# Kernel tuning notes

Measured on AMD Instinct MI355X. Metric: run time of the kernel, lower is better.

## Reference

```python
import jax, jax.numpy as jnp
import numpy as np

N = 100000      # num_nodes
E = 1600000     # num_edges (avg degree 16)
IN = 128        # in_channels
HID = 8         # hidden_channels (per head)
HEADS = 8
OUT = 64        # out_channels
NEG_SLOPE = 0.2


def setup_inputs() -> dict:
    key = jax.random.key(0)
    ks = jax.random.split(key, 11)
    s = 0.05
    return {
        "x": jax.random.normal(ks[0], (N, IN), jnp.float32),
        "edge_index": jax.random.randint(ks[1], (2, E), 0, N, dtype=jnp.int32),
        "W1": jax.random.normal(ks[2], (IN, HEADS * HID), jnp.float32) * s,
        "a_src1": jax.random.normal(ks[3], (HEADS, HID), jnp.float32) * s,
        "a_dst1": jax.random.normal(ks[4], (HEADS, HID), jnp.float32) * s,
        "b1": jnp.zeros((HEADS * HID,), jnp.float32),
        "W2": jax.random.normal(ks[5], (HEADS * HID, OUT), jnp.float32) * s,
        "a_src2": jax.random.normal(ks[6], (1, OUT), jnp.float32) * s,
        "a_dst2": jax.random.normal(ks[7], (1, OUT), jnp.float32) * s,
        "b2": jnp.zeros((OUT,), jnp.float32),
    }


def gat_conv(x, src, dst, W, a_src, a_dst, bias, heads, out_ch):
    """PyG GATConv (concat=True, dropout=0, self-loops already in src/dst)."""
    n = x.shape[0]
    h = (x @ W).reshape(n, heads, out_ch)               # [N, H, C]
    al_src = jnp.einsum('nhc,hc->nh', h, a_src)          # [N, H]
    al_dst = jnp.einsum('nhc,hc->nh', h, a_dst)          # [N, H]
    e = jax.nn.leaky_relu(al_src[src] + al_dst[dst], NEG_SLOPE)  # [E, H]
    # segment softmax over destination nodes (numerically stable)
    e_max = jax.ops.segment_max(e, dst, num_segments=n)  # [N, H]
    ex = jnp.exp(e - e_max[dst])
    denom = jax.ops.segment_sum(ex, dst, num_segments=n)
    alpha = ex / (denom[dst] + 1e-16)                    # [E, H]
    msg = h[src] * alpha[:, :, None]                     # [E, H, C]
    out = jax.ops.segment_sum(msg, dst, num_segments=n)  # [N, H, C]
    return out.reshape(n, heads * out_ch) + bias


def reference(x, edge_index, W1, a_src1, a_dst1, b1, W2, a_src2, a_dst2, b2):
    n = x.shape[0]
    loops = jnp.arange(n, dtype=edge_index.dtype)
    src = jnp.concatenate([edge_index[0], loops])        # add self-loops (PyG default)
    dst = jnp.concatenate([edge_index[1], loops])
    h = gat_conv(x, src, dst, W1, a_src1, a_dst1, b1, HEADS, HID)
    h = jax.nn.elu(h)
    out = gat_conv(h, src, dst, W2, a_src2, a_dst2, b2, 1, OUT)
    return out
```

## Files before the change

### kernel.cpp

```cpp
#include <hip/hip_runtime.h>
#include <hip/hip_bf16.h>

#define IN_CH   128
#define HEADS   8
#define HID     8
#define MID_CH  64
#define OUT_CH  64
#define CAP     64
#define NRANGE  8

typedef unsigned short u16;
__device__ __forceinline__ u16 f2bu(float f) {
    union { float f; unsigned int i; } v; v.f = f;
    unsigned int lsb = (v.i >> 16) & 1u;
    return (u16)((v.i + 0x7fffu + lsb) >> 16);
}
__device__ __forceinline__ float2 up2(unsigned int u) {
    union { unsigned int i; float f; } a, b;
    a.i = u << 16; b.i = u & 0xffff0000u;
    return make_float2(a.f, b.f);
}
__device__ __forceinline__ float lrelu(float e) { return (e > 0.f) ? e : 0.2f * e; }

__global__ __launch_bounds__(256) void k1_fill(
    const int* __restrict__ src, const int* __restrict__ dst,
    int* __restrict__ deg, int* __restrict__ adj, int E, int N) {
    int range = blockIdx.x & (NRANGE - 1);
    int chunk = blockIdx.x >> 3;
    int lo = (int)(((long long)N * range) >> 3);
    int hi = (int)(((long long)N * (range + 1)) >> 3);
    int t = chunk * 256 + threadIdx.x;
    int base = t * 4;
    if (base + 3 < E) {
        int4 d4 = *(const int4*)(dst + base);
        bool ix = (d4.x >= lo && d4.x < hi);
        bool iy = (d4.y >= lo && d4.y < hi);
        bool iz = (d4.z >= lo && d4.z < hi);
        bool iw = (d4.w >= lo && d4.w < hi);
        if (ix | iy | iz | iw) {
            int4 s4 = *(const int4*)(src + base);
            if (ix) { int p = atomicAdd(&deg[d4.x], 1); if (p < CAP) adj[d4.x * CAP + p] = s4.x; }
            if (iy) { int p = atomicAdd(&deg[d4.y], 1); if (p < CAP) adj[d4.y * CAP + p] = s4.y; }
            if (iz) { int p = atomicAdd(&deg[d4.z], 1); if (p < CAP) adj[d4.z * CAP + p] = s4.z; }
            if (iw) { int p = atomicAdd(&deg[d4.w], 1); if (p < CAP) adj[d4.w * CAP + p] = s4.w; }
        }
    } else {
        for (int j = 0; j < 4; j++) {
            int e = base + j;
            if (e < E) {
                int d = dst[e];
                if (d >= lo && d < hi) {
                    int p = atomicAdd(&deg[d], 1);
                    if (p < CAP) adj[d * CAP + p] = src[e];
                }
            }
        }
    }
}

__global__ __launch_bounds__(256) void k2_gemm1(
    const float* __restrict__ x, const float* __restrict__ W1,
    const float* __restrict__ a_src, const float* __restrict__ a_dst,
    u16* __restrict__ h1b, float* __restrict__ als, float* __restrict__ ald, int N)
{
    __shared__ float Wl[IN_CH * MID_CH];
    __shared__ float xl[16 * IN_CH];
    int tid = threadIdx.x;
    {
        const float4* W4 = (const float4*)W1;
        float4* Wl4 = (float4*)Wl;
        #pragma unroll
        for (int i = tid; i < IN_CH * MID_CH / 4; i += 256) Wl4[i] = W4[i];
    }
    int base = blockIdx.x * 16;
    {
        float4* xl4 = (float4*)xl;
        const float4* x4 = (const float4*)x;
        #pragma unroll
        for (int i = tid; i < 16 * IN_CH / 4; i += 256) {
            int r = i >> 5;
            int n = base + r;
            xl4[i] = (n < N) ? x4[(size_t)n * (IN_CH / 4) + (i & 31)]
                             : make_float4(0.f, 0.f, 0.f, 0.f);
        }
    }
    __syncthreads();

    int wave = tid >> 6, lane = tid & 63;
    int r0 = wave * 4;
    const float* xr0 = &xl[(r0 + 0) * IN_CH];
    const float* xr1 = &xl[(r0 + 1) * IN_CH];
    const float* xr2 = &xl[(r0 + 2) * IN_CH];
    const float* xr3 = &xl[(r0 + 3) * IN_CH];
    float acc0 = 0.f, acc1 = 0.f, acc2 = 0.f, acc3 = 0.f;
    #pragma unroll 8
    for (int kc = 0; kc < IN_CH; kc += 4) {
        float4 xa = *(const float4*)(xr0 + kc);
        float4 xb = *(const float4*)(xr1 + kc);
        float4 xc = *(const float4*)(xr2 + kc);
        float4 xd = *(const float4*)(xr3 + kc);
        float w0 = Wl[(kc + 0) * MID_CH + lane];
        float w1 = Wl[(kc + 1) * MID_CH + lane];
        float w2 = Wl[(kc + 2) * MID_CH + lane];
        float w3 = Wl[(kc + 3) * MID_CH + lane];
        acc0 = fmaf(xa.x, w0, acc0); acc0 = fmaf(xa.y, w1, acc0);
        acc0 = fmaf(xa.z, w2, acc0); acc0 = fmaf(xa.w, w3, acc0);
        acc1 = fmaf(xb.x, w0, acc1); acc1 = fmaf(xb.y, w1, acc1);
        acc1 = fmaf(xb.z, w2, acc1); acc1 = fmaf(xb.w, w3, acc1);
        acc2 = fmaf(xc.x, w0, acc2); acc2 = fmaf(xc.y, w1, acc2);
        acc2 = fmaf(xc.z, w2, acc2); acc2 = fmaf(xc.w, w3, acc2);
        acc3 = fmaf(xd.x, w0, acc3); acc3 = fmaf(xd.y, w1, acc3);
        acc3 = fmaf(xd.z, w2, acc3); acc3 = fmaf(xd.w, w3, acc3);
    }
    float accs[4] = {acc0, acc1, acc2, acc3};
    float asv = a_src[lane];
    float adv = a_dst[lane];
    #pragma unroll
    for (int g = 0; g < 4; g++) {
        int n = base + r0 + g;
        if (n >= N) continue;
        h1b[(size_t)n * MID_CH + lane] = f2bu(accs[g]);
        float vs = accs[g] * asv;
        float vd = accs[g] * adv;
        vs += __shfl_xor(vs, 1); vs += __shfl_xor(vs, 2); vs += __shfl_xor(vs, 4);
        vd += __shfl_xor(vd, 1); vd += __shfl_xor(vd, 2); vd += __shfl_xor(vd, 4);
        if ((lane & 7) == 0) {
            als[n * HEADS + (lane >> 3)] = vs;
            ald[n * HEADS + (lane >> 3)] = vd;
        }
    }
}

__global__ __launch_bounds__(256) void k3_agg1(
    const int* __restrict__ deg, const int* __restrict__ adj,
    const u16* __restrict__ h1b, const float* __restrict__ als,
    const float* __restrict__ ald, const float* __restrict__ b1,
    float* __restrict__ h2, int N)
{
    __shared__ int adjl[4][CAP];
    int wave = threadIdx.x >> 6, lane = threadIdx.x & 63;
    int n = blockIdx.x * 4 + wave;
    bool valid = (n < N);
    int nc = valid ? n : (N - 1);

    int g = lane >> 3;
    int c8 = lane & 7;
    int dg = deg[nc]; if (dg > CAP) dg = CAP;
    if (lane < dg) adjl[wave][lane] = adj[(size_t)nc * CAP + lane];
    float aldv = ald[nc * HEADS + c8];
    __syncthreads();

    const uint4* h1v = (const uint4*)h1b;
    float acc[8] = {0,0,0,0,0,0,0,0};
    float denom = 0.f;
    for (int i = g; i < dg; i += 8) {
        int s = adjl[wave][i];
        float ex = __expf(lrelu(als[s * HEADS + c8] + aldv));
        uint4 q = h1v[(size_t)s * 8 + c8];
        float2 p0 = up2(q.x), p1 = up2(q.y), p2 = up2(q.z), p3 = up2(q.w);
        denom += ex;
        acc[0] += ex * p0.x; acc[1] += ex * p0.y;
        acc[2] += ex * p1.x; acc[3] += ex * p1.y;
        acc[4] += ex * p2.x; acc[5] += ex * p2.y;
        acc[6] += ex * p3.x; acc[7] += ex * p3.y;
    }
    if (g == 0) {
        float ex = __expf(lrelu(als[nc * HEADS + c8] + aldv));
        uint4 q = h1v[(size_t)nc * 8 + c8];
        float2 p0 = up2(q.x), p1 = up2(q.y), p2 = up2(q.z), p3 = up2(q.w);
        denom += ex;
        acc[0] += ex * p0.x; acc[1] += ex * p0.y;
        acc[2] += ex * p1.x; acc[3] += ex * p1.y;
        acc[4] += ex * p2.x; acc[5] += ex * p2.y;
        acc[6] += ex * p3.x; acc[7] += ex * p3.y;
    }
    denom += __shfl_xor(denom, 8); denom += __shfl_xor(denom, 16); denom += __shfl_xor(denom, 32);
    #pragma unroll
    for (int j = 0; j < 8; j++) {
        acc[j] += __shfl_xor(acc[j], 8);
        acc[j] += __shfl_xor(acc[j], 16);
        acc[j] += __shfl_xor(acc[j], 32);
    }
    float inv = 1.f / (denom + 1e-16f);

    if (g == 0 && valid) {
        const float4* b4 = (const float4*)b1;
        float4 bl = b4[c8 * 2], bh = b4[c8 * 2 + 1];
        float4 o0, o1;
        o0.x = acc[0] * inv + bl.x; o0.y = acc[1] * inv + bl.y;
        o0.z = acc[2] * inv + bl.z; o0.w = acc[3] * inv + bl.w;
        o1.x = acc[4] * inv + bh.x; o1.y = acc[5] * inv + bh.y;
        o1.z = acc[6] * inv + bh.z; o1.w = acc[7] * inv + bh.w;
        o0.x = (o0.x > 0.f) ? o0.x : (__expf(o0.x) - 1.f);
        o0.y = (o0.y > 0.f) ? o0.y : (__expf(o0.y) - 1.f);
        o0.z = (o0.z > 0.f) ? o0.z : (__expf(o0.z) - 1.f);
        o0.w = (o0.w > 0.f) ? o0.w : (__expf(o0.w) - 1.f);
        o1.x = (o1.x > 0.f) ? o1.x : (__expf(o1.x) - 1.f);
        o1.y = (o1.y > 0.f) ? o1.y : (__expf(o1.y) - 1.f);
        o1.z = (o1.z > 0.f) ? o1.z : (__expf(o1.z) - 1.f);
        o1.w = (o1.w > 0.f) ? o1.w : (__expf(o1.w) - 1.f);
        float4* h2v = (float4*)h2;
        h2v[(size_t)n * 16 + c8 * 2]     = o0;
        h2v[(size_t)n * 16 + c8 * 2 + 1] = o1;
    }
}

__global__ __launch_bounds__(256) void k4_gemm2(
    const float* __restrict__ h2, const float* __restrict__ W2,
    const float* __restrict__ a_src, const float* __restrict__ a_dst,
    u16* __restrict__ t2b, float* __restrict__ als, float* __restrict__ ald, int N)
{
    __shared__ float Wl[MID_CH * OUT_CH];
    __shared__ float xl[16 * MID_CH];
    int tid = threadIdx.x;
    {
        const float4* W4 = (const float4*)W2;
        float4* Wl4 = (float4*)Wl;
        #pragma unroll
        for (int i = tid; i < MID_CH * OUT_CH / 4; i += 256) Wl4[i] = W4[i];
    }
    int base = blockIdx.x * 16;
    {
        float4* xl4 = (float4*)xl;
        const float4* x4 = (const float4*)h2;
        #pragma unroll
        for (int i = tid; i < 16 * MID_CH / 4; i += 256) {
            int r = i >> 4;
            int n = base + r;
            xl4[i] = (n < N) ? x4[(size_t)n * (MID_CH / 4) + (i & 15)]
                             : make_float4(0.f, 0.f, 0.f, 0.f);
        }
    }
    __syncthreads();

    int wave = tid >> 6, lane = tid & 63;
    int r0 = wave * 4;
    const float* xr0 = &xl[(r0 + 0) * MID_CH];
    const float* xr1 = &xl[(r0 + 1) * MID_CH];
    const float* xr2 = &xl[(r0 + 2) * MID_CH];
    const float* xr3 = &xl[(r0 + 3) * MID_CH];
    float acc0 = 0.f, acc1 = 0.f, acc2 = 0.f, acc3 = 0.f;
    #pragma unroll 8
    for (int kc = 0; kc < MID_CH; kc += 4) {
        float4 xa = *(const float4*)(xr0 + kc);
        float4 xb = *(const float4*)(xr1 + kc);
        float4 xc = *(const float4*)(xr2 + kc);
        float4 xd = *(const float4*)(xr3 + kc);
        float w0 = Wl[(kc + 0) * OUT_CH + lane];
        float w1 = Wl[(kc + 1) * OUT_CH + lane];
        float w2 = Wl[(kc + 2) * OUT_CH + lane];
        float w3 = Wl[(kc + 3) * OUT_CH + lane];
        acc0 = fmaf(xa.x, w0, acc0); acc0 = fmaf(xa.y, w1, acc0);
        acc0 = fmaf(xa.z, w2, acc0); acc0 = fmaf(xa.w, w3, acc0);
        acc1 = fmaf(xb.x, w0, acc1); acc1 = fmaf(xb.y, w1, acc1);
        acc1 = fmaf(xb.z, w2, acc1); acc1 = fmaf(xb.w, w3, acc1);
        acc2 = fmaf(xc.x, w0, acc2); acc2 = fmaf(xc.y, w1, acc2);
        acc2 = fmaf(xc.z, w2, acc2); acc2 = fmaf(xc.w, w3, acc2);
        acc3 = fmaf(xd.x, w0, acc3); acc3 = fmaf(xd.y, w1, acc3);
        acc3 = fmaf(xd.z, w2, acc3); acc3 = fmaf(xd.w, w3, acc3);
    }
    float accs[4] = {acc0, acc1, acc2, acc3};
    float asv = a_src[lane];
    float adv = a_dst[lane];
    #pragma unroll
    for (int g = 0; g < 4; g++) {
        int n = base + r0 + g;
        if (n >= N) continue;
        t2b[(size_t)n * OUT_CH + lane] = f2bu(accs[g]);
        float vs = accs[g] * asv;
        float vd = accs[g] * adv;
        #pragma unroll
        for (int off = 1; off < 64; off <<= 1) {
            vs += __shfl_xor(vs, off);
            vd += __shfl_xor(vd, off);
        }
        if (lane == 0) { als[n] = vs; ald[n] = vd; }
    }
}

__global__ __launch_bounds__(256) void k5_agg2(
    const int* __restrict__ deg, const int* __restrict__ adj,
    const u16* __restrict__ t2b, const float* __restrict__ als,
    const float* __restrict__ ald, const float* __restrict__ b2,
    float* __restrict__ out, int N)
{
    __shared__ int adjl[4][CAP];
    int wave = threadIdx.x >> 6, lane = threadIdx.x & 63;
    int n = blockIdx.x * 4 + wave;
    bool valid = (n < N);
    int nc = valid ? n : (N - 1);

    int g = lane >> 3;
    int c8 = lane & 7;
    int dg = deg[nc]; if (dg > CAP) dg = CAP;
    if (lane < dg) adjl[wave][lane] = adj[(size_t)nc * CAP + lane];
    float aldv = ald[nc];
    __syncthreads();

    const uint4* t2v = (const uint4*)t2b;
    float acc[8] = {0,0,0,0,0,0,0,0};
    float denom = 0.f;
    for (int i = g; i < dg; i += 8) {
        int s = adjl[wave][i];
        float ex = __expf(lrelu(als[s] + aldv));
        uint4 q = t2v[(size_t)s * 8 + c8];
        float2 p0 = up2(q.x), p1 = up2(q.y), p2 = up2(q.z), p3 = up2(q.w);
        denom += ex;
        acc[0] += ex * p0.x; acc[1] += ex * p0.y;
        acc[2] += ex * p1.x; acc[3] += ex * p1.y;
        acc[4] += ex * p2.x; acc[5] += ex * p2.y;
        acc[6] += ex * p3.x; acc[7] += ex * p3.y;
    }
    if (g == 0) {
        float ex = __expf(lrelu(als[nc] + aldv));
        uint4 q = t2v[(size_t)nc * 8 + c8];
        float2 p0 = up2(q.x), p1 = up2(q.y), p2 = up2(q.z), p3 = up2(q.w);
        denom += ex;
        acc[0] += ex * p0.x; acc[1] += ex * p0.y;
        acc[2] += ex * p1.x; acc[3] += ex * p1.y;
        acc[4] += ex * p2.x; acc[5] += ex * p2.y;
        acc[6] += ex * p3.x; acc[7] += ex * p3.y;
    }
    denom += __shfl_xor(denom, 8); denom += __shfl_xor(denom, 16); denom += __shfl_xor(denom, 32);
    #pragma unroll
    for (int j = 0; j < 8; j++) {
        acc[j] += __shfl_xor(acc[j], 8);
        acc[j] += __shfl_xor(acc[j], 16);
        acc[j] += __shfl_xor(acc[j], 32);
    }
    float inv = 1.f / (denom + 1e-16f);

    if (g == 0 && valid) {
        const float4* b4 = (const float4*)b2;
        float4 bl = b4[c8 * 2], bh = b4[c8 * 2 + 1];
        float4 o0, o1;
        o0.x = acc[0] * inv + bl.x; o0.y = acc[1] * inv + bl.y;
        o0.z = acc[2] * inv + bl.z; o0.w = acc[3] * inv + bl.w;
        o1.x = acc[4] * inv + bh.x; o1.y = acc[5] * inv + bh.y;
        o1.z = acc[6] * inv + bh.z; o1.w = acc[7] * inv + bh.w;
        float4* ov = (float4*)out;
        ov[(size_t)n * 16 + c8 * 2]     = o0;
        ov[(size_t)n * 16 + c8 * 2 + 1] = o1;
    }
}

extern "C" void kernel_launch(void* const* d_in, const int* in_sizes, int n_in,
                              void* d_out, int out_size, void* d_ws, size_t ws_size,
                              hipStream_t stream) {
    const float* x   = (const float*)d_in[0];
    const int*   ei  = (const int*)d_in[1];
    const float* W1  = (const float*)d_in[2];
    const float* as1 = (const float*)d_in[3];
    const float* ad1 = (const float*)d_in[4];
    const float* b1  = (const float*)d_in[5];
    const float* W2  = (const float*)d_in[6];
    const float* as2 = (const float*)d_in[7];
    const float* ad2 = (const float*)d_in[8];
    const float* b2  = (const float*)d_in[9];
    float* out = (float*)d_out;

    int N = in_sizes[0] / IN_CH;
    int E = in_sizes[1] / 2;
    const int* srcp = ei;
    const int* dstp = ei + E;

    char* w = (char*)d_ws;
    size_t off = 0;
    auto alloc = [&](size_t bytes) {
        void* p = w + off;
        off += (bytes + 255) & ~(size_t)255;
        return p;
    };
    int*   deg  = (int*)  alloc((size_t)N * 4);
    int*   adj  = (int*)  alloc((size_t)N * CAP * 4);
    u16*   h1b  = (u16*)  alloc((size_t)N * MID_CH * 2);
    float* als1 = (float*)alloc((size_t)N * HEADS * 4);
    float* ald1 = (float*)alloc((size_t)N * HEADS * 4);
    float* h2   = (float*)alloc((size_t)N * MID_CH * 4);
    u16*   t2b  = (u16*)  alloc((size_t)N * OUT_CH * 2);
    float* als2 = (float*)alloc((size_t)N * 4);
    float* ald2 = (float*)alloc((size_t)N * 4);
    (void)ws_size; (void)n_in; (void)out_size;

    hipMemsetAsync(deg, 0, (size_t)N * 4, stream);
    int chunks = (E + 1023) / 1024;
    k1_fill<<<chunks * NRANGE, 256, 0, stream>>>(srcp, dstp, deg, adj, E, N);
    k2_gemm1<<<(N + 15) / 16, 256, 0, stream>>>(x, W1, as1, ad1, h1b, als1, ald1, N);
    k3_agg1<<<(N + 3) / 4, 256, 0, stream>>>(deg, adj, h1b, als1, ald1, b1, h2, N);
    k4_gemm2<<<(N + 15) / 16, 256, 0, stream>>>(h2, W2, as2, ad2, t2b, als2, ald2, N);
    k5_agg2<<<(N + 3) / 4, 256, 0, stream>>>(deg, adj, t2b, als2, ald2, b2, out, N);
}
```

Baseline: 370.3 us.

## Fuse adjacency fill into first GEMM kernel to overlap atomics with loads

Merges the edge-bucketing fill kernel into the layer-1 GEMM kernel. Each block handles two fill units: it issues the dst/src loads and the degree atomics before staging W1 and x into shared memory, then writes the adjacency entries afterwards, so atomic latency overlaps with the GEMM loads and one launch is removed. The grid is enlarged when needed to cover all fill units, and launch bounds now request 4 blocks per SM. This adds register pressure and relies on the GEMM path guarding blocks whose rows fall past N.

```diff
diff --git a/kernel.cpp b/kernel.cpp
--- a/kernel.cpp
+++ b/kernel.cpp
@@ -22,57 +22,77 @@
 }
 __device__ __forceinline__ float lrelu(float e) { return (e > 0.f) ? e : 0.2f * e; }
 
-__global__ __launch_bounds__(256) void k1_fill(
+#define FILL_ISSUE(U, D4, S4, P4)                                              \
+    do {                                                                        \
+        int range_ = (U) & (NRANGE - 1);                                        \
+        int chunk_ = (U) >> 3;                                                  \
+        int lo_ = (int)(((long long)N * range_) >> 3);                          \
+        int hi_ = (int)(((long long)N * (range_ + 1)) >> 3);                    \
+        int base_ = (chunk_ * 256 + threadIdx.x) * 4;                           \
+        if (base_ + 3 < E) {                                                    \
+            D4 = *(const int4*)(dst + base_);                                   \
+            bool ix_ = (D4.x >= lo_ && D4.x < hi_);                             \
+            bool iy_ = (D4.y >= lo_ && D4.y < hi_);                             \
+            bool iz_ = (D4.z >= lo_ && D4.z < hi_);                             \
+            bool iw_ = (D4.w >= lo_ && D4.w < hi_);                             \
+            if (ix_ | iy_ | iz_ | iw_) {                                        \
+                S4 = *(const int4*)(src + base_);                               \
+                if (ix_) P4.x = atomicAdd(&deg[D4.x], 1);                       \
+                if (iy_) P4.y = atomicAdd(&deg[D4.y], 1);                       \
+                if (iz_) P4.z = atomicAdd(&deg[D4.z], 1);                       \
+                if (iw_) P4.w = atomicAdd(&deg[D4.w], 1);                       \
+            }                                                                   \
+        } else {                                                                \
+            for (int j_ = 0; j_ < 4; j_++) {                                    \
+                int e_ = base_ + j_;                                            \
+                if (e_ < E) {                                                   \
+                    int d_ = dst[e_];                                           \
+                    if (d_ >= lo_ && d_ < hi_) {                                \
+                        int p_ = atomicAdd(&deg[d_], 1);                        \
+                        if (p_ < CAP) adj[(size_t)d_ * CAP + p_] = src[e_];     \
+                    }                                                           \
+                }                                                               \
+            }                                                                   \
+        }                                                                       \
+    } while (0)
+
+#define FILL_STORE(D4, S4, P4)                                                  \
+    do {                                                                        \
+        if (P4.x < CAP) adj[(size_t)D4.x * CAP + P4.x] = S4.x;                  \
+        if (P4.y < CAP) adj[(size_t)D4.y * CAP + P4.y] = S4.y;                  \
+        if (P4.z < CAP) adj[(size_t)D4.z * CAP + P4.z] = S4.z;                  \
+        if (P4.w < CAP) adj[(size_t)D4.w * CAP + P4.w] = S4.w;                  \
+    } while (0)
+
+__global__ __launch_bounds__(256, 4) void k12_fillgemm(
     const int* __restrict__ src, const int* __restrict__ dst,
-    int* __restrict__ deg, int* __restrict__ adj, int E, int N) {
-    int range = blockIdx.x & (NRANGE - 1);
-    int chunk = blockIdx.x >> 3;
-    int lo = (int)(((long long)N * range) >> 3);
-    int hi = (int)(((long long)N * (range + 1)) >> 3);
-    int t = chunk * 256 + threadIdx.x;
-    int base = t * 4;
-    if (base + 3 < E) {
-        int4 d4 = *(const int4*)(dst + base);
-        bool ix = (d4.x >= lo && d4.x < hi);
-        bool iy = (d4.y >= lo && d4.y < hi);
-        bool iz = (d4.z >= lo && d4.z < hi);
-        bool iw = (d4.w >= lo && d4.w < hi);
-        if (ix | iy | iz | iw) {
-            int4 s4 = *(const int4*)(src + base);
-            if (ix) { int p = atomicAdd(&deg[d4.x], 1); if (p < CAP) adj[d4.x * CAP + p] = s4.x; }
-            if (iy) { int p = atomicAdd(&deg[d4.y], 1); if (p < CAP) adj[d4.y * CAP + p] = s4.y; }
-            if (iz) { int p = atomicAdd(&deg[d4.z], 1); if (p < CAP) adj[d4.z * CAP + p] = s4.z; }
-            if (iw) { int p = atomicAdd(&deg[d4.w], 1); if (p < CAP) adj[d4.w * CAP + p] = s4.w; }
-        }
-    } else {
-        for (int j = 0; j < 4; j++) {
-            int e = base + j;
-            if (e < E) {
-                int d = dst[e];
-                if (d >= lo && d < hi) {
-                    int p = atomicAdd(&deg[d], 1);
-                    if (p < CAP) adj[d * CAP + p] = src[e];
-                }
-            }
-        }
-    }
-}
-
-__global__ __launch_bounds__(256) void k2_gemm1(
+    int* __restrict__ deg, int* __restrict__ adj,
     const float* __restrict__ x, const float* __restrict__ W1,
     const float* __restrict__ a_src, const float* __restrict__ a_dst,
-    u16* __restrict__ h1b, float* __restrict__ als, float* __restrict__ ald, int N)
+    u16* __restrict__ h1b, float* __restrict__ als, float* __restrict__ ald,
+    int E, int N, int grid, int nUnits)
 {
     __shared__ float Wl[IN_CH * MID_CH];
     __shared__ float xl[16 * IN_CH];
     int tid = threadIdx.x;
+    int bid = blockIdx.x;
+
+    int4 dA = make_int4(0, 0, 0, 0), sA = make_int4(0, 0, 0, 0);
+    int4 pA = make_int4(CAP, CAP, CAP, CAP);
+    int4 dB = make_int4(0, 0, 0, 0), sB = make_int4(0, 0, 0, 0);
+    int4 pB = make_int4(CAP, CAP, CAP, CAP);
+    int uA = bid;
+    int uB = bid + grid;
+    if (uA < nUnits) FILL_ISSUE(uA, dA, sA, pA);
+    if (uB < nUnits) FILL_ISSUE(uB, dB, sB, pB);
+
     {
         const float4* W4 = (const float4*)W1;
         float4* Wl4 = (float4*)Wl;
         #pragma unroll
         for (int i = tid; i < IN_CH * MID_CH / 4; i += 256) Wl4[i] = W4[i];
     }
-    int base = blockIdx.x * 16;
+    int base = bid * 16;
     {
         float4* xl4 = (float4*)xl;
         const float4* x4 = (const float4*)x;
@@ -84,6 +104,9 @@
                              : make_float4(0.f, 0.f, 0.f, 0.f);
         }
     }
+
+    FILL_STORE(dA, sA, pA);
+    FILL_STORE(dB, sB, pB);
     __syncthreads();
 
     int wave = tid >> 6, lane = tid & 63;
@@ -383,9 +406,15 @@
     (void)ws_size; (void)n_in; (void)out_size;
 
     hipMemsetAsync(deg, 0, (size_t)N * 4, stream);
+
     int chunks = (E + 1023) / 1024;
-    k1_fill<<<chunks * NRANGE, 256, 0, stream>>>(srcp, dstp, deg, adj, E, N);
-    k2_gemm1<<<(N + 15) / 16, 256, 0, stream>>>(x, W1, as1, ad1, h1b, als1, ald1, N);
+    int nUnits = chunks * NRANGE;
+    int ngemm  = (N + 15) / 16;
+    int grid   = ngemm;
+    if (grid * 2 < nUnits) grid = (nUnits + 1) / 2;
+    k12_fillgemm<<<grid, 256, 0, stream>>>(srcp, dstp, deg, adj,
+                                           x, W1, as1, ad1, h1b, als1, ald1,
+                                           E, N, grid, nUnits);
     k3_agg1<<<(N + 3) / 4, 256, 0, stream>>>(deg, adj, h1b, als1, ald1, b1, h2, N);
     k4_gemm2<<<(N + 15) / 16, 256, 0, stream>>>(h2, W2, as2, ad2, t2b, als2, ald2, N);
     k5_agg2<<<(N + 3) / 4, 256, 0, stream>>>(deg, adj, t2b, als2, ald2, b2, out, N);
```

Result: no change. 363.1 us (-2.0%).
